# Optimization experiments

Measured on AMD Instinct MI355X. Metric: run time of the kernel, lower is better.

The kernel has to match this reference:

```python
import jax, jax.numpy as jnp
import numpy as np

B, N, D, OUT = 2048, 118, 64, 64


def setup_inputs() -> dict:
    key = jax.random.key(0)
    ks = jax.random.split(key, 16)
    inp = {}
    inp["e"] = jax.random.normal(ks[0], (B, N, D), jnp.float32)
    inp["f"] = jax.random.normal(ks[1], (B, N, D), jnp.float32)
    inp["k1"] = jax.random.normal(ks[2], (B, N, N), jnp.float32)
    inp["k2"] = jax.random.normal(ks[3], (B, N, N), jnp.float32)
    inp["G_ndiag"] = jax.random.normal(ks[4], (B, N, N), jnp.float32)
    inp["B_ndiag"] = jax.random.normal(ks[5], (B, N, N), jnp.float32)
    # keep diagonal admittances away from 0 so G^2+B^2 is well-conditioned
    inp["G_diag"] = jax.random.uniform(ks[6], (B, N, 1), jnp.float32) + 0.5
    inp["B_diag"] = jax.random.uniform(ks[7], (B, N, 1), jnp.float32) + 0.5
    inp["Pd"] = jax.random.normal(ks[8], (B, N, 1), jnp.float32)
    inp["Qd"] = jax.random.normal(ks[9], (B, N, 1), jnp.float32)
    s_in = 1.0 / np.sqrt(5 * D)
    inp["W1"] = jax.random.normal(ks[10], (5 * D, OUT), jnp.float32) * s_in
    inp["b1"] = jnp.zeros((OUT,), jnp.float32)
    inp["W2"] = jax.random.normal(ks[11], (5 * D, OUT), jnp.float32) * s_in
    inp["b2"] = jnp.zeros((OUT,), jnp.float32)
    s_a = 1.0 / np.sqrt(D)
    inp["wae"] = jax.random.normal(ks[12], (D, 1), jnp.float32) * s_a
    inp["bae"] = jnp.zeros((1,), jnp.float32)
    inp["waf"] = jax.random.normal(ks[13], (D, 1), jnp.float32) * s_a
    inp["baf"] = jnp.zeros((1,), jnp.float32)
    return inp


def _att(x, w, b):
    # mean-pool over nodes (axis -2, keepdims) then linear+sigmoid -> [B,1,1]
    pooled = jnp.mean(x, axis=-2, keepdims=True)
    return jax.nn.sigmoid(pooled @ w + b)


def reference(e, f, k1, k2, G_ndiag, B_ndiag, G_diag, B_diag, Pd, Qd,
              W1, b1, W2, b2, wae, bae, waf, baf):
    base = e * e + f * f + 0.1
    Ge = G_ndiag @ e
    Gf = G_ndiag @ f
    Be = B_ndiag @ e
    Bf = B_ndiag @ f
    alpha = Pd * e / base + Qd * f / base - Ge - Bf
    # NOTE: original code uses bmm(B_ndiag, f) here (not Be) -- kept faithful
    beta = Qd * e / base - Pd * f / base + Gf + Bf
    base_gb = G_diag * G_diag + B_diag * B_diag
    e3 = (alpha * G_diag + beta * B_diag) / base_gb
    f3 = (beta * G_diag - alpha * B_diag) / base_gb
    base1 = Ge - Bf
    base2 = Gf + Be
    ef2 = e * e + f * f
    Pt = Pd - ef2 * G_diag
    Qt = Qd + ef2 * B_diag
    new_e = (Pt * base1 + Qt * base2) / base_gb
    new_f = (Pt * base2 - Qt * base1) / base_gb
    e1 = k1 @ e
    f1 = k1 @ f
    e2 = k2 @ e
    f2 = k2 @ f
    a1 = _att(e3, wae, bae)
    a2 = _att(new_e, wae, bae)
    a3 = _att(e1, wae, bae)
    a4 = _att(e2, wae, bae)
    a_base = a1 + a2 + a3 + a4 + 0.0001
    e_new = jnp.concatenate(
        ((a1 / a_base) * e3, (a2 / a_base) * new_e,
         (a3 / a_base) * e1, (a4 / a_base) * e2, e), axis=2)
    b1a = _att(f3, waf, baf)
    b2a = _att(new_f, waf, baf)
    b3a = _att(f1, waf, baf)
    b4a = _att(f2, waf, baf)
    b_base = b1a + b2a + b3a + b4a + 0.0001
    f_new = jnp.concatenate(
        ((b1a / b_base) * f3, (b2a / b_base) * new_f,
         (b3a / b_base) * f1, (b4a / b_base) * f2, f), axis=2)
    e_out = jax.nn.relu(e_new @ W1 + b1)
    f_out = jax.nn.relu(f_new @ W2 + b2)
    return (e_out, f_out)
```

## Files before the change

### kernel.cpp

```cpp
#include <hip/hip_runtime.h>
#include <stdint.h>

#define NB 118
#define MSZ (118*118)
#define S 136

typedef _Float16 f16x8 __attribute__((ext_vector_type(8)));
typedef _Float16 f16x4 __attribute__((ext_vector_type(4)));
typedef float f32x4 __attribute__((ext_vector_type(4)));

__device__ __forceinline__ f32x4 mfma16(f16x8 a, f16x8 b, f32x4 c) {
    return __builtin_amdgcn_mfma_f32_16x16x32_f16(a, b, c, 0, 0, 0);
}

__global__ __launch_bounds__(256) void prep_w(const float* __restrict__ W1,
                                              const float* __restrict__ W2,
                                              _Float16* __restrict__ WP)
{
    int g = blockIdx.x * 256 + threadIdx.x;
    if (g >= 5120) return;
    int wsel = g / 2560;
    int r = g % 2560;
    int t = r >> 8;
    int c = (r >> 6) & 3;
    int l = r & 63;
    const float* W = wsel ? W2 : W1;
    _Float16* dst = WP + wsel * 20480 + r * 8;
#pragma unroll
    for (int j = 0; j < 8; j++) {
        int kk = t * 32 + (l >> 4) * 8 + j;
        int col = c * 16 + (l & 15);
        dst[j] = (_Float16)W[kk * 64 + col];
    }
}

__device__ __forceinline__ void stage1(const float* __restrict__ M,
                                       const _Float16* SH_, int w, int lane,
                                       f32x4 (&acc)[8])
{
    const int l15 = lane & 15, lhi = lane >> 4;
    int row = w * 16 + l15;
    if (row > 117) row = 117;
    const float* __restrict__ pr_ = M + row * NB;
#pragma unroll
    for (int t = 0; t < 4; t++) {
        int kb = t * 32 + lhi * 8;
        const float* p = pr_ + kb;
        float vv[8];
        if (t < 3) {
#pragma unroll
            for (int q = 0; q < 4; q++) {
                float2 u = *(const float2*)(p + 2 * q);
                vv[2 * q] = u.x; vv[2 * q + 1] = u.y;
            }
        } else {
#pragma unroll
            for (int q = 0; q < 4; q++) {
                int k0 = kb + 2 * q;
                if (k0 <= 116) {
                    float2 u = *(const float2*)(p + 2 * q);
                    vv[2 * q] = u.x; vv[2 * q + 1] = u.y;
                } else { vv[2 * q] = 0.f; vv[2 * q + 1] = 0.f; }
            }
        }
        f16x8 a;
#pragma unroll
        for (int j = 0; j < 8; j++) a[j] = (_Float16)vv[j];
#pragma unroll
        for (int c = 0; c < 8; c++) {
            f16x8 bfr = *(const f16x8*)&SH_[(c * 16 + l15) * S + t * 32 + lhi * 8];
            acc[c] = mfma16(a, bfr, acc[c]);
        }
    }
}

__device__ __forceinline__ void writeRT(_Float16* RT_, const f16x4 (&pE)[4],
                                        const f16x4 (&pF)[4],
                                        float sE, float sF, int w, int lane)
{
    const int l15 = lane & 15, lhi = lane >> 4;
    const _Float16 hE = (_Float16)sE, hF = (_Float16)sF;
#pragma unroll
    for (int c = 0; c < 4; c++)
#pragma unroll
        for (int r = 0; r < 4; r++) {
            int row = w * 16 + lhi * 4 + r;
            RT_[row * S + c * 16 + l15]      = pE[c][r] * hE;
            RT_[row * S + 64 + c * 16 + l15] = pF[c][r] * hF;
        }
}

__device__ __forceinline__ void s2round(const _Float16* RT_,
                                        const _Float16* __restrict__ W1P,
                                        const _Float16* __restrict__ W2P,
                                        int j, int w, int lane,
                                        f32x4 (&VE)[4], f32x4 (&VF)[4])
{
    const int l15 = lane & 15, lhi = lane >> 4;
    const int row = w * 16 + l15;
#pragma unroll
    for (int th = 0; th < 2; th++) {
        int t = 2 * j + th;
        int kk = th * 32 + lhi * 8;
        f16x8 ae = *(const f16x8*)&RT_[row * S + kk];
        f16x8 af = *(const f16x8*)&RT_[row * S + 64 + kk];
#pragma unroll
        for (int c = 0; c < 4; c++) {
            f16x8 bw1 = *(const f16x8*)&W1P[((t * 4 + c) * 64 + lane) * 8];
            f16x8 bw2 = *(const f16x8*)&W2P[((t * 4 + c) * 64 + lane) * 8];
            VE[c] = mfma16(ae, bw1, VE[c]);
            VF[c] = mfma16(af, bw2, VF[c]);
        }
    }
}

__global__ __launch_bounds__(512, 2) void gcn_main(
    const float* __restrict__ E, const float* __restrict__ F,
    const float* __restrict__ K1, const float* __restrict__ K2,
    const float* __restrict__ Gn, const float* __restrict__ Bn,
    const float* __restrict__ Gdg, const float* __restrict__ Bdg,
    const float* __restrict__ Pdg, const float* __restrict__ Qdg,
    const float* __restrict__ b1, const float* __restrict__ b2,
    const float* __restrict__ wae, const float* __restrict__ bae,
    const float* __restrict__ waf, const float* __restrict__ baf,
    const _Float16* __restrict__ W1P, const _Float16* __restrict__ W2P,
    float* __restrict__ outE, float* __restrict__ outF)
{
    __shared__ __align__(16) _Float16 SH[128 * S];
    __shared__ float cs[8][64];
    __shared__ float sPd[128], sQd[128], sGd[128], sBd[128];

    const int b = blockIdx.x;
    const int tid = threadIdx.x;
    const int lane = tid & 63;
    const int w = tid >> 6;
    const int l15 = lane & 15;
    const int lhi = lane >> 4;
    const f32x4 Z4 = {0.f, 0.f, 0.f, 0.f};

    ((float*)cs)[tid] = 0.0f;
    if (tid < 128) {
        f16x8 z8 = {};
        *(f16x8*)&SH[tid * S + 120] = z8;
    }
    if (tid < NB) {
        sPd[tid] = Pdg[b * NB + tid]; sQd[tid] = Qdg[b * NB + tid];
        sGd[tid] = Gdg[b * NB + tid]; sBd[tid] = Bdg[b * NB + tid];
    } else if (tid < 128) {
        sPd[tid] = 0.f; sQd[tid] = 0.f; sGd[tid] = 1.f; sBd[tid] = 1.f;
    }

    const float* eb = E + (size_t)b * NB * 64;
    const float* fb = F + (size_t)b * NB * 64;
    for (int id = tid; id < 960; id += 512) {
        int m = id >= 480;
        int r = id - (m ? 480 : 0);
        int q = r >> 4;
        int dq = r & 15;
        const float* src = m ? fb : eb;
        int dbase = m ? 64 : 0;
        f32x4 v0, v1, v2, v3;
        int row = 4 * q;
        v0 = *(const f32x4*)(src + (row + 0) * 64 + dq * 4);
        v1 = *(const f32x4*)(src + (row + 1) * 64 + dq * 4);
        v2 = (row + 2 < NB) ? *(const f32x4*)(src + (row + 2) * 64 + dq * 4) : Z4;
        v3 = (row + 3 < NB) ? *(const f32x4*)(src + (row + 3) * 64 + dq * 4) : Z4;
#pragma unroll
        for (int j = 0; j < 4; j++) {
            f16x4 t = { (_Float16)v0[j], (_Float16)v1[j], (_Float16)v2[j], (_Float16)v3[j] };
            *(f16x4*)&SH[(dbase + dq * 4 + j) * S + 4 * q] = t;
        }
    }
    __syncthreads();

    f32x4 accA[8], accB_[8];
#pragma unroll
    for (int c = 0; c < 8; c++) { accA[c] = Z4; accB_[c] = Z4; }
    stage1(Gn + (size_t)b * MSZ, SH, w, lane, accA);
    stage1(Bn + (size_t)b * MSZ, SH, w, lane, accB_);

    f16x4 p0E[4], p0F[4], p1E[4], p1F[4];
#pragma unroll
    for (int c = 0; c < 4; c++) {
        float se3 = 0, sf3 = 0, sne = 0, snf = 0;
#pragma unroll
        for (int r = 0; r < 4; r++) {
            int row = w * 16 + lhi * 4 + r;
            int d = c * 16 + l15;
            float Ge = accA[c][r], Gf = accA[c + 4][r];
            float Be = accB_[c][r], Bf = accB_[c + 4][r];
            float ev = (float)SH[d * S + row];
            float fv = (float)SH[(64 + d) * S + row];
            float pd = sPd[row], qd = sQd[row], gd = sGd[row], bd = sBd[row];
            float ef2 = ev * ev + fv * fv;
            float ib = 1.0f / (ef2 + 0.1f);
            float alpha = (pd * ev + qd * fv) * ib - Ge - Bf;
            float beta  = (qd * ev - pd * fv) * ib + Gf + Bf;
            float ibg = 1.0f / (gd * gd + bd * bd);
            float e3 = (alpha * gd + beta * bd) * ibg;
            float f3 = (beta * gd - alpha * bd) * ibg;
            float bs1 = Ge - Bf, bs2 = Gf + Be;
            float Pt = pd - ef2 * gd, Qt = qd + ef2 * bd;
            float ne = (Pt * bs1 + Qt * bs2) * ibg;
            float nf = (Pt * bs2 - Qt * bs1) * ibg;
            p0E[c][r] = (_Float16)e3; p0F[c][r] = (_Float16)f3;
            p1E[c][r] = (_Float16)ne; p1F[c][r] = (_Float16)nf;
            if (row < NB) { se3 += e3; sf3 += f3; sne += ne; snf += nf; }
        }
        se3 += __shfl_xor(se3, 16); se3 += __shfl_xor(se3, 32);
        sf3 += __shfl_xor(sf3, 16); sf3 += __shfl_xor(sf3, 32);
        sne += __shfl_xor(sne, 16); sne += __shfl_xor(sne, 32);
        snf += __shfl_xor(snf, 16); snf += __shfl_xor(snf, 32);
        if (lhi == 0) {
            atomicAdd(&cs[0][c * 16 + l15], se3);
            atomicAdd(&cs[4][c * 16 + l15], sf3);
            atomicAdd(&cs[1][c * 16 + l15], sne);
            atomicAdd(&cs[5][c * 16 + l15], snf);
        }
    }

    f16x4 p2E[4], p2F[4], p3E[4], p3F[4];
    {
        f32x4 accK[8];
#pragma unroll
        for (int c = 0; c < 8; c++) accK[c] = Z4;
        stage1(K1 + (size_t)b * MSZ, SH, w, lane, accK);
#pragma unroll
        for (int c = 0; c < 4; c++) {
            float sE = 0, sF = 0;
#pragma unroll
            for (int r = 0; r < 4; r++) {
                int row = w * 16 + lhi * 4 + r;
                float ve = accK[c][r], vf = accK[c + 4][r];
                p2E[c][r] = (_Float16)ve; p2F[c][r] = (_Float16)vf;
                if (row < NB) { sE += ve; sF += vf; }
            }
            sE += __shfl_xor(sE, 16); sE += __shfl_xor(sE, 32);
            sF += __shfl_xor(sF, 16); sF += __shfl_xor(sF, 32);
            if (lhi == 0) {
                atomicAdd(&cs[2][c * 16 + l15], sE);
                atomicAdd(&cs[6][c * 16 + l15], sF);
            }
        }
#pragma unroll
        for (int c = 0; c < 8; c++) accK[c] = Z4;
        stage1(K2 + (size_t)b * MSZ, SH, w, lane, accK);
#pragma unroll
        for (int c = 0; c < 4; c++) {
            float sE = 0, sF = 0;
#pragma unroll
            for (int r = 0; r < 4; r++) {
                int row = w * 16 + lhi * 4 + r;
                float ve = accK[c][r], vf = accK[c + 4][r];
                p3E[c][r] = (_Float16)ve; p3F[c][r] = (_Float16)vf;
                if (row < NB) { sE += ve; sF += vf; }
            }
            sE += __shfl_xor(sE, 16); sE += __shfl_xor(sE, 32);
            sF += __shfl_xor(sF, 16); sF += __shfl_xor(sF, 32);
            if (lhi == 0) {
                atomicAdd(&cs[3][c * 16 + l15], sE);
                atomicAdd(&cs[7][c * 16 + l15], sF);
            }
        }
    }
    __syncthreads();

    float sEs[4], sFs[4];
    {
        float wl_e = wae[lane], wl_f = waf[lane];
        float b_e = bae[0], b_f = baf[0];
        float aE[4], aF[4];
#pragma unroll
        for (int s2 = 0; s2 < 4; s2++) {
            float xe = cs[s2][lane] * wl_e;
            float xf = cs[4 + s2][lane] * wl_f;
#pragma unroll
            for (int m = 1; m < 64; m <<= 1) { xe += __shfl_xor(xe, m); xf += __shfl_xor(xf, m); }
            aE[s2] = 1.0f / (1.0f + __expf(-(xe * (1.0f / NB) + b_e)));
            aF[s2] = 1.0f / (1.0f + __expf(-(xf * (1.0f / NB) + b_f)));
        }
        float ebs = aE[0] + aE[1] + aE[2] + aE[3] + 1e-4f;
        float fbs = aF[0] + aF[1] + aF[2] + aF[3] + 1e-4f;
#pragma unroll
        for (int j = 0; j < 4; j++) { sEs[j] = aE[j] / ebs; sFs[j] = aF[j] / fbs; }
    }

    f32x4 VE[4], VF[4];
#pragma unroll
    for (int c = 0; c < 4; c++) { VE[c] = Z4; VF[c] = Z4; }

    writeRT(SH, p0E, p0F, sEs[0], sFs[0], w, lane);
    s2round(SH, W1P, W2P, 0, w, lane, VE, VF);
    writeRT(SH, p1E, p1F, sEs[1], sFs[1], w, lane);
    s2round(SH, W1P, W2P, 1, w, lane, VE, VF);
    writeRT(SH, p2E, p2F, sEs[2], sFs[2], w, lane);
    s2round(SH, W1P, W2P, 2, w, lane, VE, VF);
    writeRT(SH, p3E, p3F, sEs[3], sFs[3], w, lane);
    s2round(SH, W1P, W2P, 3, w, lane, VE, VF);

#pragma unroll
    for (int th = 0; th < 2; th++) {
        int t = 8 + th;
        int row = w * 16 + l15;
        if (row > 117) row = 117;
        const float* pe = eb + row * 64 + th * 32 + lhi * 8;
        const float* pf = fb + row * 64 + th * 32 + lhi * 8;
        f32x4 q0 = *(const f32x4*)pe, q1 = *(const f32x4*)(pe + 4);
        f32x4 u0 = *(const f32x4*)pf, u1 = *(const f32x4*)(pf + 4);
        f16x8 ae, af;
#pragma unroll
        for (int jj = 0; jj < 4; jj++) {
            ae[jj] = (_Float16)q0[jj]; ae[4 + jj] = (_Float16)q1[jj];
            af[jj] = (_Float16)u0[jj]; af[4 + jj] = (_Float16)u1[jj];
        }
#pragma unroll
        for (int c = 0; c < 4; c++) {
            f16x8 bw1 = *(const f16x8*)&W1P[((t * 4 + c) * 64 + lane) * 8];
            f16x8 bw2 = *(const f16x8*)&W2P[((t * 4 + c) * 64 + lane) * 8];
            VE[c] = mfma16(ae, bw1, VE[c]);
            VF[c] = mfma16(af, bw2, VF[c]);
        }
    }

#pragma unroll
    for (int c = 0; c < 4; c++) {
        float bb1 = b1[c * 16 + l15];
        float bb2 = b2[c * 16 + l15];
#pragma unroll
        for (int r = 0; r < 4; r++) {
            int row = w * 16 + lhi * 4 + r;
            if (row < NB) {
                size_t o = ((size_t)b * NB + row) * 64 + c * 16 + l15;
                outE[o] = fmaxf(VE[c][r] + bb1, 0.0f);
                outF[o] = fmaxf(VF[c][r] + bb2, 0.0f);
            }
        }
    }
}

extern "C" void kernel_launch(void* const* d_in, const int* in_sizes, int n_in,
                              void* d_out, int out_size, void* d_ws, size_t ws_size,
                              hipStream_t stream)
{
    (void)in_sizes; (void)n_in; (void)out_size; (void)ws_size;
    const float* E   = (const float*)d_in[0];
    const float* F   = (const float*)d_in[1];
    const float* K1  = (const float*)d_in[2];
    const float* K2  = (const float*)d_in[3];
    const float* Gn  = (const float*)d_in[4];
    const float* Bn  = (const float*)d_in[5];
    const float* Gdg = (const float*)d_in[6];
    const float* Bdg = (const float*)d_in[7];
    const float* Pdg = (const float*)d_in[8];
    const float* Qdg = (const float*)d_in[9];
    const float* W1  = (const float*)d_in[10];
    const float* b1  = (const float*)d_in[11];
    const float* W2  = (const float*)d_in[12];
    const float* b2  = (const float*)d_in[13];
    const float* wae = (const float*)d_in[14];
    const float* bae = (const float*)d_in[15];
    const float* waf = (const float*)d_in[16];
    const float* baf = (const float*)d_in[17];

    _Float16* WP = (_Float16*)d_ws;
    float* outE = (float*)d_out;
    float* outF = outE + (size_t)2048 * NB * 64;

    prep_w<<<20, 256, 0, stream>>>(W1, W2, WP);
    gcn_main<<<2048, 512, 0, stream>>>(E, F, K1, K2, Gn, Bn, Gdg, Bdg, Pdg, Qdg,
                                       b1, b2, wae, bae, waf, baf,
                                       WP, WP + 20480, outE, outF);
}
```

Before: 299.6 us.

## Prefetch adjacency matrices into LDS with async global_load_lds double buffers

Adds two large LDS buffers and issues asynchronous global-to-LDS loads for G_ndiag/B_ndiag at kernel start, then for K1/K2 while the elementwise alpha/beta stage runs. stage1 now reads matrix rows from LDS instead of global memory. The goal is to hide global latency of the 118x118 matrix loads behind other work. In exchange, LDS use per block grows to roughly 150 KB, which likely allows only one block per CU instead of two, and two extra barriers are added.

```diff
diff --git a/kernel.cpp b/kernel.cpp
--- a/kernel.cpp
+++ b/kernel.cpp
@@ -3,6 +3,8 @@
 
 #define NB 118
 #define MSZ (118*118)
+#define KCH 3584
+#define KFL (KCH*4)
 #define S 136
 
 typedef _Float16 f16x8 __attribute__((ext_vector_type(8)));
@@ -34,14 +36,31 @@
     }
 }
 
-__device__ __forceinline__ void stage1(const float* __restrict__ M,
+__device__ __forceinline__ void prefetchK(const float* src, float* dst,
+                                          int w, int lane)
+{
+#pragma unroll
+    for (int i = 0; i < 7; i++) {
+        int chunk = w * 448 + i * 64 + lane;
+        int fidx = chunk * 4;
+        if (fidx > MSZ - 4) fidx = MSZ - 4;
+        const float* g = src + fidx;
+        float* l = dst + (w * 448 + i * 64) * 4;
+        __builtin_amdgcn_global_load_lds(
+            (const __attribute__((address_space(1))) void*)g,
+            (__attribute__((address_space(3))) void*)l,
+            16, 0, 0);
+    }
+}
+
+__device__ __forceinline__ void stage1(const float* M,
                                        const _Float16* SH_, int w, int lane,
                                        f32x4 (&acc)[8])
 {
     const int l15 = lane & 15, lhi = lane >> 4;
     int row = w * 16 + l15;
     if (row > 117) row = 117;
-    const float* __restrict__ pr_ = M + row * NB;
+    const float* pr_ = M + row * NB;
 #pragma unroll
     for (int t = 0; t < 4; t++) {
         int kb = t * 32 + lhi * 8;
@@ -127,6 +146,8 @@
     float* __restrict__ outE, float* __restrict__ outF)
 {
     __shared__ __align__(16) _Float16 SH[128 * S];
+    __shared__ __align__(16) float KAf[KFL];
+    __shared__ __align__(16) float KBf[KFL];
     __shared__ float cs[8][64];
     __shared__ float sPd[128], sQd[128], sGd[128], sBd[128];
 
@@ -137,6 +158,9 @@
     const int l15 = lane & 15;
     const int lhi = lane >> 4;
     const f32x4 Z4 = {0.f, 0.f, 0.f, 0.f};
+
+    prefetchK(Gn + (size_t)b * MSZ, KAf, w, lane);
+    prefetchK(Bn + (size_t)b * MSZ, KBf, w, lane);
 
     ((float*)cs)[tid] = 0.0f;
     if (tid < 128) {
@@ -176,8 +200,12 @@
     f32x4 accA[8], accB_[8];
 #pragma unroll
     for (int c = 0; c < 8; c++) { accA[c] = Z4; accB_[c] = Z4; }
-    stage1(Gn + (size_t)b * MSZ, SH, w, lane, accA);
-    stage1(Bn + (size_t)b * MSZ, SH, w, lane, accB_);
+    stage1(KAf, SH, w, lane, accA);
+    stage1(KBf, SH, w, lane, accB_);
+    __syncthreads();
+
+    prefetchK(K1 + (size_t)b * MSZ, KAf, w, lane);
+    prefetchK(K2 + (size_t)b * MSZ, KBf, w, lane);
 
     f16x4 p0E[4], p0F[4], p1E[4], p1F[4];
 #pragma unroll
@@ -218,13 +246,14 @@
             atomicAdd(&cs[5][c * 16 + l15], snf);
         }
     }
+    __syncthreads();
 
     f16x4 p2E[4], p2F[4], p3E[4], p3F[4];
     {
         f32x4 accK[8];
 #pragma unroll
         for (int c = 0; c < 8; c++) accK[c] = Z4;
-        stage1(K1 + (size_t)b * MSZ, SH, w, lane, accK);
+        stage1(KAf, SH, w, lane, accK);
 #pragma unroll
         for (int c = 0; c < 4; c++) {
             float sE = 0, sF = 0;
@@ -244,7 +273,7 @@
         }
 #pragma unroll
         for (int c = 0; c < 8; c++) accK[c] = Z4;
-        stage1(K2 + (size_t)b * MSZ, SH, w, lane, accK);
+        stage1(KBf, SH, w, lane, accK);
 #pragma unroll
         for (int c = 0; c < 4; c++) {
             float sE = 0, sF = 0;
```

After: 277.5 us. 1.08x faster.
